# Performance work log

Hardware: AMD Instinct MI355X
Metric: run time of the kernel (lower is better)

Reference implementation:

```python
import jax, jax.numpy as jnp
import numpy as np

NUM_HEADS = 16
NEG_INF = -1e30


def setup_inputs() -> dict:
    key = jax.random.key(0)
    ks = jax.random.split(key, 12)
    T, B, E = 1024, 8, 1024
    H = NUM_HEADS
    hd = E // H
    gain = 1.0 / np.sqrt(2.0)
    # xavier_uniform bound for [E, E] weight
    bound = np.sqrt(6.0 / (E + E))
    inp = {
        "query": jax.random.normal(ks[0], (T, B, E), jnp.float32),
        "key": jax.random.normal(ks[1], (T, B, E), jnp.float32),
        "value": jax.random.normal(ks[2], (T, B, E), jnp.float32),
        "key_padding_mask": jnp.zeros((B, T), dtype=bool),  # no padding
        "attn_mask": jnp.triu(jnp.ones((T, T), dtype=bool), k=1),  # causal
        "Wq": jax.random.uniform(ks[3], (E, E), jnp.float32, -bound * gain, bound * gain),
        "bq": jnp.zeros((E,), jnp.float32),
        "Wk": jax.random.uniform(ks[4], (E, E), jnp.float32, -bound * gain, bound * gain),
        "bk": jnp.zeros((E,), jnp.float32),
        "Wv": jax.random.uniform(ks[5], (E, E), jnp.float32, -bound * gain, bound * gain),
        "bv": jnp.zeros((E,), jnp.float32),
        "Wo": jax.random.uniform(ks[6], (E, E), jnp.float32, -bound, bound),
        "bo": jnp.zeros((E,), jnp.float32),
    }
    return inp


def reference(query, key, value, key_padding_mask, attn_mask,
              Wq, bq, Wk, bk, Wv, bv, Wo, bo):
    T, B, E = query.shape
    H = NUM_HEADS
    hd = E // H
    scaling = hd ** -0.5
    S = key.shape[0]

    # projections (nn.Linear: x @ W.T + b)
    q = (query @ Wq.T + bq) * scaling          # [T, B, E]
    k = key @ Wk.T + bk                         # [S, B, E]
    v = value @ Wv.T + bv                       # [S, B, E]

    # -> [B*H, len, hd] (fairseq layout)
    q = q.reshape(T, B * H, hd).transpose(1, 0, 2)
    k = k.reshape(S, B * H, hd).transpose(1, 0, 2)
    v = v.reshape(S, B * H, hd).transpose(1, 0, 2)

    scores = jnp.einsum('nth,nsh->nts', q, k)   # [B*H, T, S]
    scores = jnp.where(attn_mask[None, :, :], NEG_INF, scores)
    scores = scores.reshape(B, H, T, S)
    scores = jnp.where(key_padding_mask[:, None, None, :], NEG_INF, scores)

    # fp32 softmax (matches softmax(..., dtype=torch.float32))
    weights = jax.nn.softmax(scores.astype(jnp.float32), axis=-1)  # [B, H, T, S]

    # dropout p=0.0 in eval -> identity
    probs = weights.reshape(B * H, T, S)
    attn = jnp.einsum('nts,nsh->nth', probs, v)  # [B*H, T, hd]
    attn = attn.transpose(1, 0, 2).reshape(T, B, E)
    attn = attn @ Wo.T + bo                      # [T, B, E]

    avg_weights = jnp.sum(weights, axis=1) / H   # [B, T, S]
    return attn, avg_weights, weights
```

## Files before the change

### kernel.cpp

```cpp
#include <hip/hip_runtime.h>
#include <hip/hip_bf16.h>
#include <stdint.h>

typedef unsigned short u16;
typedef __attribute__((ext_vector_type(8))) short bf16x8;
typedef __attribute__((ext_vector_type(4))) float f32x4;

#define LDS_AS __attribute__((address_space(3)))
#define GLB_AS __attribute__((address_space(1)))


__device__ __forceinline__ u16 f2bf(float f) {
  union { float f; uint32_t u; } v; v.f = f;
  uint32_t u = v.u;
  u += 0x7FFFu + ((u >> 16) & 1u);
  return (u16)(u >> 16);
}

__device__ __forceinline__ f32x4 mfma16(bf16x8 a, bf16x8 b, f32x4 c) {
  return __builtin_amdgcn_mfma_f32_16x16x32_bf16(a, b, c, 0, 0, 0);
}

__device__ __forceinline__ void gll16(const void* g, void* l) {
  __builtin_amdgcn_global_load_lds((const GLB_AS void*)(uintptr_t)g,
                                   (LDS_AS void*)(uintptr_t)l, 16, 0, 0);
}

__global__ __launch_bounds__(256) void k_cvt_all(
    const float* __restrict__ a0, const float* __restrict__ a1, const float* __restrict__ a2,
    const float* __restrict__ w0, const float* __restrict__ w1,
    const float* __restrict__ w2, const float* __restrict__ w3,
    u16* __restrict__ da0, u16* __restrict__ da1, u16* __restrict__ da2,
    u16* __restrict__ dw0, u16* __restrict__ dw1, u16* __restrict__ dw2, u16* __restrict__ dw3)
{
  int gid = blockIdx.x;
  const float* s; u16* d; int idx;
  if (gid < 24576) {
    int seg = gid >> 13; idx = gid & 8191;
    s = seg == 0 ? a0 : (seg == 1 ? a1 : a2);
    d = seg == 0 ? da0 : (seg == 1 ? da1 : da2);
  } else {
    int g2 = gid - 24576;
    int seg = g2 >> 10; idx = g2 & 1023;
    s = seg == 0 ? w0 : (seg == 1 ? w1 : (seg == 2 ? w2 : w3));
    d = seg == 0 ? dw0 : (seg == 1 ? dw1 : (seg == 2 ? dw2 : dw3));
  }
  int i = (idx * 256 + threadIdx.x) * 4;
  float4 v = *reinterpret_cast<const float4*>(s + i);
  ushort4 o;
  o.x = f2bf(v.x); o.y = f2bf(v.y); o.z = f2bf(v.z); o.w = f2bf(v.w);
  *reinterpret_cast<ushort4*>(d + i) = o;
}

__device__ __forceinline__ void gemm_core(
    const u16* __restrict__ A, const u16* __restrict__ Bw,
    const float* __restrict__ bias, void* __restrict__ outp,
    float scale, bool fp32out)
{
  __shared__ u16 aLds[128 * 64];
  __shared__ u16 bLds[128 * 64];
  const int tid = threadIdx.x;
  const int w = tid >> 6, lane = tid & 63;
  const int fr = lane & 15, fh = lane >> 4;
  const int m0 = blockIdx.x * 128, n0 = blockIdx.y * 128;
  const int wr = w >> 1, wc = w & 1;
  const int srow = tid >> 3, scol = (tid & 7) * 8;

  f32x4 zero4 = {0.f, 0.f, 0.f, 0.f};
  f32x4 acc[4][4];
#pragma unroll
  for (int i = 0; i < 4; i++)
#pragma unroll
    for (int j = 0; j < 4; j++) acc[i][j] = zero4;

  const u16* ag = A + (size_t)(m0 + srow) * 1024 + scol;
  const u16* bg = Bw + (size_t)(n0 + srow) * 1024 + scol;

  for (int k0 = 0; k0 < 1024; k0 += 64) {
#pragma unroll
    for (int it = 0; it < 4; ++it) {
      gll16(ag + (size_t)it * 32 * 1024 + k0, aLds + it * 2048 + w * 512);
      gll16(bg + (size_t)it * 32 * 1024 + k0, bLds + it * 2048 + w * 512);
    }
    __syncthreads();
#pragma unroll
    for (int ks = 0; ks < 2; ++ks) {
      bf16x8 af[4], bfr[4];
#pragma unroll
      for (int mi = 0; mi < 4; mi++)
        af[mi] = *reinterpret_cast<const bf16x8*>(&aLds[(wr * 64 + mi * 16 + fr) * 64 + ks * 32 + fh * 8]);
#pragma unroll
      for (int nj = 0; nj < 4; nj++)
        bfr[nj] = *reinterpret_cast<const bf16x8*>(&bLds[(wc * 64 + nj * 16 + fr) * 64 + ks * 32 + fh * 8]);
#pragma unroll
      for (int mi = 0; mi < 4; mi++)
#pragma unroll
        for (int nj = 0; nj < 4; nj++)
          acc[mi][nj] = mfma16(af[mi], bfr[nj], acc[mi][nj]);
    }
    __syncthreads();
  }

#pragma unroll
  for (int nj = 0; nj < 4; nj++) {
    int j = n0 + wc * 64 + nj * 16 + fr;
    float bj = bias[j];
#pragma unroll
    for (int mi = 0; mi < 4; mi++) {
#pragma unroll
      for (int r = 0; r < 4; r++) {
        int i = m0 + wr * 64 + mi * 16 + fh * 4 + r;
        float v = acc[mi][nj][r] + bj;
        if (fp32out) {
          ((float*)outp)[(size_t)i * 1024 + j] = v;
        } else {
          v *= scale;
          int t = i >> 3, b = i & 7;
          int h = j >> 6, d = j & 63;
          ((u16*)outp)[((size_t)((b * 16 + h) * 1024 + t)) * 64 + d] = f2bf(v);
        }
      }
    }
  }
}

__global__ __launch_bounds__(256) void k_gemm_qkv(
    const u16* __restrict__ xq, const u16* __restrict__ xk, const u16* __restrict__ xv,
    const u16* __restrict__ wq, const u16* __restrict__ wk, const u16* __restrict__ wv,
    const float* __restrict__ bq, const float* __restrict__ bk, const float* __restrict__ bv,
    u16* __restrict__ qo, u16* __restrict__ ko, u16* __restrict__ vo)
{
  int z = blockIdx.z;
  const u16* A = z == 0 ? xq : (z == 1 ? xk : xv);
  const u16* Bw = z == 0 ? wq : (z == 1 ? wk : wv);
  const float* bias = z == 0 ? bq : (z == 1 ? bk : bv);
  u16* o = z == 0 ? qo : (z == 1 ? ko : vo);
  float scale = z == 0 ? 0.125f : 1.0f;
  gemm_core(A, Bw, bias, o, scale, false);
}

__global__ __launch_bounds__(256) void k_gemm_o(
    const u16* __restrict__ A, const u16* __restrict__ Bw,
    const float* __restrict__ bias, float* __restrict__ outp)
{
  gemm_core(A, Bw, bias, outp, 1.0f, true);
}

__global__ __launch_bounds__(256) void k_transpose(const u16* __restrict__ vb, u16* __restrict__ vt) {
  __shared__ u16 tile[64][72];
  int n = blockIdx.y, t0 = blockIdx.x * 64;
  int tid = threadIdx.x;
  int r = tid >> 2, c0 = (tid & 3) * 16;
  const u16* src = vb + ((size_t)n * 1024 + t0 + r) * 64 + c0;
#pragma unroll
  for (int ii = 0; ii < 16; ++ii) tile[c0 + ii][r] = src[ii];
  __syncthreads();
  int d = tid >> 2;
  u16* dst = vt + ((size_t)(n * 64) + d) * 1024 + t0 + c0;
  *reinterpret_cast<uint4*>(dst)     = *reinterpret_cast<const uint4*>(&tile[d][c0]);
  *reinterpret_cast<uint4*>(dst + 8) = *reinterpret_cast<const uint4*>(&tile[d][c0 + 8]);
}

__device__ __forceinline__ void attn_step(
    const u16* lds_k, u16* lds_p, const bf16x8 (&vf)[2][4],
    int sb, int tb_, int w, int fr, int fh,
    bf16x8 qf0, bf16x8 qf1,
    f32x4 (&oacc)[4], float (&m4)[4], float (&l4)[4])
{
  int t0 = tb_ * 64 + w * 16;
  f32x4 dd[4];
#pragma unroll
  for (int ss = 0; ss < 4; ++ss) {
    int row = ss * 16 + fr;
    const u16* kr = lds_k + row * 64;
    int c0 = (fh * 16) ^ ((row & 7) << 4);
    int c1 = (64 + fh * 16) ^ ((row & 7) << 4);
    bf16x8 kf0 = *reinterpret_cast<const bf16x8*>(kr + (c0 >> 1));
    bf16x8 kf1 = *reinterpret_cast<const bf16x8*>(kr + (c1 >> 1));
    f32x4 z = {0.f, 0.f, 0.f, 0.f};
    z = mfma16(qf0, kf0, z);
    dd[ss] = mfma16(qf1, kf1, z);
  }
  if (sb == tb_) {
#pragma unroll
    for (int ss = 0; ss < 4; ++ss) {
      int s_c = sb * 64 + ss * 16 + fr;
#pragma unroll
      for (int r = 0; r < 4; ++r)
        if (s_c > t0 + fh * 4 + r) dd[ss][r] = -3.0e38f;
    }
  }
  float mn[4], scale[4];
#pragma unroll
  for (int r = 0; r < 4; ++r) {
    float bm = fmaxf(fmaxf(dd[0][r], dd[1][r]), fmaxf(dd[2][r], dd[3][r]));
#pragma unroll
    for (int bmk = 1; bmk < 16; bmk <<= 1)
      bm = fmaxf(bm, __shfl_xor(bm, bmk, 64));
    mn[r] = fmaxf(m4[r], bm);
    scale[r] = __expf(m4[r] - mn[r]);
    m4[r] = mn[r];
  }
#pragma unroll
  for (int ss = 0; ss < 4; ++ss) {
#pragma unroll
    for (int r = 0; r < 4; ++r) {
      float p = __expf(dd[ss][r] - mn[r]);
      dd[ss][r] = p;
      int row = fh * 4 + r;
      int cb = ((ss * 16 + fr) * 2) ^ ((row & 7) << 4);
      lds_p[row * 64 + (cb >> 1)] = f2bf(p);
    }
  }
#pragma unroll
  for (int r = 0; r < 4; ++r) {
    float s = (dd[0][r] + dd[1][r]) + (dd[2][r] + dd[3][r]);
#pragma unroll
    for (int bmk = 1; bmk < 16; bmk <<= 1)
      s += __shfl_xor(s, bmk, 64);
    l4[r] = l4[r] * scale[r] + s;
#pragma unroll
    for (int db = 0; db < 4; ++db) oacc[db][r] *= scale[r];
  }
  asm volatile("s_waitcnt lgkmcnt(0)" ::: "memory");
  __builtin_amdgcn_sched_barrier(0);
#pragma unroll
  for (int ks = 0; ks < 2; ++ks) {
    int pc = (ks * 64 + fh * 16) ^ ((fr & 7) << 4);
    bf16x8 pa = *reinterpret_cast<const bf16x8*>(lds_p + fr * 64 + (pc >> 1));
#pragma unroll
    for (int db = 0; db < 4; ++db)
      oacc[db] = mfma16(pa, vf[ks][db], oacc[db]);
  }
}

__global__ __launch_bounds__(256) void k_attn(
    const u16* __restrict__ qb, const u16* __restrict__ kb, const u16* __restrict__ vt,
    float* __restrict__ m_ws, float* __restrict__ l_ws, u16* __restrict__ attn_pre)
{
  __shared__ u16 kT[2][64 * 64];
  __shared__ u16 pT[4][16 * 64];
  int tid = threadIdx.x, w = tid >> 6, lane = tid & 63;
  int fr = lane & 15, fh = lane >> 4;
  int n = blockIdx.x, j = blockIdx.y;
  int tbH = 15 - j, tbL = j;
  const u16* kb_n = kb + (size_t)n * 1024 * 64;
  const u16* vt_n = vt + (size_t)n * 64 * 1024;

  bf16x8 qfH0, qfH1, qfL0, qfL1;
  {
    const u16* q = qb + ((size_t)n * 1024 + tbH * 64 + w * 16 + fr) * 64;
    qfH0 = *reinterpret_cast<const bf16x8*>(q + fh * 8);
    qfH1 = *reinterpret_cast<const bf16x8*>(q + 32 + fh * 8);
    q = qb + ((size_t)n * 1024 + tbL * 64 + w * 16 + fr) * 64;
    qfL0 = *reinterpret_cast<const bf16x8*>(q + fh * 8);
    qfL1 = *reinterpret_cast<const bf16x8*>(q + 32 + fh * 8);
  }
  f32x4 oaccH[4], oaccL[4];
  float mH[4], lH[4], mL[4], lL[4];
#pragma unroll
  for (int i = 0; i < 4; ++i) {
    oaccH[i] = (f32x4){0.f, 0.f, 0.f, 0.f};
    oaccL[i] = (f32x4){0.f, 0.f, 0.f, 0.f};
    mH[i] = -3.0e38f; lH[i] = 0.f; mL[i] = -3.0e38f; lL[i] = 0.f;
  }

  auto stage = [&](int buf, int sb) {
#pragma unroll
    for (int it = 0; it < 2; ++it) {
      int rbase = w * 16 + it * 8;
      int row = rbase + (lane >> 3);
      int colb = ((lane & 7) * 16) ^ ((lane >> 3) << 4);
      const u16* src = kb_n + ((size_t)(sb * 64 + row)) * 64 + (colb >> 1);
      gll16(src, &kT[buf][rbase * 64]);
    }
  };

  stage(0, 0);
  asm volatile("s_waitcnt vmcnt(0)" ::: "memory");
  __syncthreads();
  int cur = 0;
  for (int sb = 0; sb <= tbH; ++sb) {
    if (sb < tbH) stage(cur ^ 1, sb + 1);
    bf16x8 vf[2][4];
#pragma unroll
    for (int ks = 0; ks < 2; ++ks)
#pragma unroll
      for (int db = 0; db < 4; ++db)
        vf[ks][db] = *reinterpret_cast<const bf16x8*>(
            vt_n + ((size_t)(db * 16 + fr)) * 1024 + sb * 64 + ks * 32 + fh * 8);
    attn_step(kT[cur], pT[w], vf, sb, tbH, w, fr, fh, qfH0, qfH1, oaccH, mH, lH);
    if (sb <= tbL)
      attn_step(kT[cur], pT[w], vf, sb, tbL, w, fr, fh, qfL0, qfL1, oaccL, mL, lL);
    asm volatile("s_waitcnt vmcnt(0)" ::: "memory");
    __syncthreads();
    cur ^= 1;
  }

  int b_ = n >> 4, h_ = n & 15;
  {
    int t0 = tbH * 64 + w * 16;
    if (fr == 0) {
#pragma unroll
      for (int r = 0; r < 4; ++r) {
        m_ws[n * 1024 + t0 + fh * 4 + r] = mH[r];
        l_ws[n * 1024 + t0 + fh * 4 + r] = lH[r];
      }
    }
#pragma unroll
    for (int db = 0; db < 4; ++db)
#pragma unroll
      for (int r = 0; r < 4; ++r)
        attn_pre[((size_t)((t0 + fh * 4 + r) * 8 + b_)) * 1024 + h_ * 64 + db * 16 + fr] =
            f2bf(oaccH[db][r] / lH[r]);
  }
  {
    int t0 = tbL * 64 + w * 16;
    if (fr == 0) {
#pragma unroll
      for (int r = 0; r < 4; ++r) {
        m_ws[n * 1024 + t0 + fh * 4 + r] = mL[r];
        l_ws[n * 1024 + t0 + fh * 4 + r] = lL[r];
      }
    }
#pragma unroll
    for (int db = 0; db < 4; ++db)
#pragma unroll
      for (int r = 0; r < 4; ++r)
        attn_pre[((size_t)((t0 + fh * 4 + r) * 8 + b_)) * 1024 + h_ * 64 + db * 16 + fr] =
            f2bf(oaccL[db][r] / lL[r]);
  }
}

__global__ __launch_bounds__(512) void k_weights(
    const u16* __restrict__ qb, const u16* __restrict__ kb,
    const float* __restrict__ m_ws, const float* __restrict__ l_ws,
    float* __restrict__ wout, float* __restrict__ avg)
{
  __shared__ u16 kT[2][512 * 64];
  const float L2E = 1.4426950408889634f;
  int pid = blockIdx.x;
  int b = pid >> 5, pr = pid & 31;
  int tid = threadIdx.x;
  int w = tid >> 6, lane = tid & 63, fr = lane & 15, fh = lane >> 4;
  f32x4 zero4 = {0.f, 0.f, 0.f, 0.f};

  int pA = pr, pB = 63 - pr;
  int t0A = pA * 16, t0B = pB * 16;

  f32x4 avgA[8], avgB[8];
#pragma unroll
  for (int i = 0; i < 8; ++i) { avgA[i] = zero4; avgB[i] = zero4; }

  const int srow8 = lane >> 3;
  const int scolb = ((lane & 7) * 16) ^ (srow8 << 4);

  auto stage = [&](int buf, int cc) {
    const u16* kb_n = kb + (size_t)(b * 16 + (cc >> 1)) * 65536;
    int base = (cc & 1) * 512;
#pragma unroll
    for (int j = 0; j < 8; ++j) {
      int rbase = j * 64 + w * 8;
      const u16* src = kb_n + ((size_t)(base + rbase + srow8)) * 64 + (scolb >> 1);
      gll16(src, &kT[buf][rbase * 64]);
    }
  };

  stage(0, 0);
  int cur = 0;

  for (int h = 0; h < 16; ++h) {
    int n = b * 16 + h;
    const u16* qrA = qb + ((size_t)n * 1024 + t0A + fr) * 64;
    const u16* qrB = qb + ((size_t)n * 1024 + t0B + fr) * 64;
    bf16x8 qA0 = *reinterpret_cast<const bf16x8*>(qrA + fh * 8);
    bf16x8 qA1 = *reinterpret_cast<const bf16x8*>(qrA + 32 + fh * 8);
    bf16x8 qB0 = *reinterpret_cast<const bf16x8*>(qrB + fh * 8);
    bf16x8 qB1 = *reinterpret_cast<const bf16x8*>(qrB + 32 + fh * 8);
    float cA = -m_ws[n * 1024 + t0A + fr] * L2E - __log2f(l_ws[n * 1024 + t0A + fr]);
    float cB = -m_ws[n * 1024 + t0B + fr] * L2E - __log2f(l_ws[n * 1024 + t0B + fr]);
    float* wrowA = wout + ((size_t)n << 20) + ((size_t)t0A << 10);
    float* wrowB = wout + ((size_t)n << 20) + ((size_t)t0B << 10);

#pragma unroll
    for (int kh = 0; kh < 2; ++kh) {
      int cc = h * 2 + kh;
      __builtin_amdgcn_s_barrier();
      __builtin_amdgcn_sched_barrier(0);
      if (cc < 31) stage(cur ^ 1, cc + 1);
      __builtin_amdgcn_sched_barrier(0);
      asm volatile("s_waitcnt vmcnt(8)" ::: "memory");
      __builtin_amdgcn_s_barrier();
      __builtin_amdgcn_sched_barrier(0);

      const u16* kbuf_l = kT[cur];
#pragma unroll
      for (int i = 0; i < 4; ++i) {
        int sl = w + 8 * i;
        int sg = kh * 32 + sl;
        int rowl = sl * 16 + fr;
        const u16* kr = &kbuf_l[rowl * 64];
        int c0 = (fh * 16) ^ ((rowl & 7) << 4);
        int c1 = (64 + fh * 16) ^ ((rowl & 7) << 4);
        bf16x8 kf0 = *reinterpret_cast<const bf16x8*>(kr + (c0 >> 1));
        bf16x8 kf1 = *reinterpret_cast<const bf16x8*>(kr + (c1 >> 1));

        {
          f32x4 dd = zero4;
          dd = mfma16(kf0, qA0, dd);
          dd = mfma16(kf1, qA1, dd);
          f32x4 wv;
#pragma unroll
          for (int rr = 0; rr < 4; ++rr) {
            bool valid = (sg < pA) | ((sg == pA) & (fh * 4 + rr <= fr));
            wv[rr] = valid ? __builtin_amdgcn_exp2f(dd[rr] * L2E + cA) : 0.f;
          }
          avgA[kh * 4 + i] += wv;
          *reinterpret_cast<f32x4*>(wrowA + (size_t)fr * 1024 + sg * 16 + fh * 4) = wv;
        }
        {
          f32x4 dd = zero4;
          dd = mfma16(kf0, qB0, dd);
          dd = mfma16(kf1, qB1, dd);
          f32x4 wv;
#pragma unroll
          for (int rr = 0; rr < 4; ++rr) {
            bool valid = (sg < pB) | ((sg == pB) & (fh * 4 + rr <= fr));
            wv[rr] = valid ? __builtin_amdgcn_exp2f(dd[rr] * L2E + cB) : 0.f;
          }
          avgB[kh * 4 + i] += wv;
          *reinterpret_cast<f32x4*>(wrowB + (size_t)fr * 1024 + sg * 16 + fh * 4) = wv;
        }
      }
      cur ^= 1;
    }
  }

  float* arowA = avg + (((size_t)b << 10) + t0A) * 1024;
  float* arowB = avg + (((size_t)b << 10) + t0B) * 1024;
#pragma unroll
  for (int i = 0; i < 8; ++i) {
    int sg = (i >> 2) * 32 + (w + 8 * (i & 3));
    f32x4 vA = avgA[i], vB = avgB[i];
#pragma unroll
    for (int rr = 0; rr < 4; ++rr) { vA[rr] *= 0.0625f; vB[rr] *= 0.0625f; }
    *reinterpret_cast<f32x4*>(arowA + (size_t)fr * 1024 + sg * 16 + fh * 4) = vA;
    *reinterpret_cast<f32x4*>(arowB + (size_t)fr * 1024 + sg * 16 + fh * 4) = vB;
  }
}

extern "C" void kernel_launch(void* const* d_in, const int* in_sizes, int n_in,
                              void* d_out, int out_size, void* d_ws, size_t ws_size,
                              hipStream_t stream)
{
  const float* query = (const float*)d_in[0];
  const float* key_  = (const float*)d_in[1];
  const float* value = (const float*)d_in[2];
  const float* Wq = (const float*)d_in[5];
  const float* bq = (const float*)d_in[6];
  const float* Wk = (const float*)d_in[7];
  const float* bk = (const float*)d_in[8];
  const float* Wv = (const float*)d_in[9];
  const float* bv = (const float*)d_in[10];
  const float* Wo = (const float*)d_in[11];
  const float* bo = (const float*)d_in[12];

  char* ws = (char*)d_ws;
  size_t off = 0;
  auto alloc = [&](size_t bytes) { char* p = ws + off; off += (bytes + 255) & ~255ull; return p; };

  u16* xq   = (u16*)alloc(8192ull * 1024 * 2);
  u16* xk   = (u16*)alloc(8192ull * 1024 * 2);
  u16* xv   = (u16*)alloc(8192ull * 1024 * 2);
  u16* wqb  = (u16*)alloc(1024ull * 1024 * 2);
  u16* wkb  = (u16*)alloc(1024ull * 1024 * 2);
  u16* wvb  = (u16*)alloc(1024ull * 1024 * 2);
  u16* wob  = (u16*)alloc(1024ull * 1024 * 2);
  u16* qbuf = (u16*)alloc(128ull * 1024 * 64 * 2);
  u16* kbuf = (u16*)alloc(128ull * 1024 * 64 * 2);
  u16* vbuf = (u16*)alloc(128ull * 1024 * 64 * 2);
  u16* vtb  = (u16*)alloc(128ull * 64 * 1024 * 2);
  u16* apre = (u16*)alloc(8192ull * 1024 * 2);
  float* mws = (float*)alloc(128ull * 1024 * 4);
  float* lws = (float*)alloc(128ull * 1024 * 4);

  float* out_attn = (float*)d_out;
  float* out_avg  = out_attn + 8388608;
  float* out_w    = out_avg + 8388608;

  k_cvt_all<<<28672, 256, 0, stream>>>(query, key_, value, Wq, Wk, Wv, Wo,
                                       xq, xk, xv, wqb, wkb, wvb, wob);

  k_gemm_qkv<<<dim3(64, 8, 3), 256, 0, stream>>>(xq, xk, xv, wqb, wkb, wvb,
                                                 bq, bk, bv, qbuf, kbuf, vbuf);

  k_transpose<<<dim3(16, 128), 256, 0, stream>>>(vbuf, vtb);
  k_attn<<<dim3(128, 8), 256, 0, stream>>>(qbuf, kbuf, vtb, mws, lws, apre);
  k_weights<<<256, 512, 0, stream>>>(qbuf, kbuf, mws, lws, out_w, out_avg);
  k_gemm_o<<<dim3(64, 8), 256, 0, stream>>>(apre, wob, bo, out_attn);
}
```

Measured before the change: 408.8 us.

## Split weights kernel to one query tile per block and pipeline attn K staging

k_weights now gives each block a single 16-row query tile instead of a balanced pair, and doubles the grid to 512 blocks. K is staged in 256-row quarters with a smaller LDS footprint, and the vmcnt waits are tuned to match. Separately, k_attn replaces its full vmcnt(0)+syncthreads at the end of each iteration with barrier/partial-wait double buffering, so the next K block loads while the current one is computed. The weights kernel still computes all 1024 key columns per row, so the old causal load-balance pairing is unnecessary. More blocks raise occupancy, but each block now re-stages K once per query tile, which doubles K reads.

Measured after the change: 453.5 us. +10.9%, slower.

```diff
diff --git a/kernel.cpp b/kernel.cpp
--- a/kernel.cpp
+++ b/kernel.cpp
@@ -277,11 +277,8 @@
   };
 
   stage(0, 0);
-  asm volatile("s_waitcnt vmcnt(0)" ::: "memory");
-  __syncthreads();
   int cur = 0;
   for (int sb = 0; sb <= tbH; ++sb) {
-    if (sb < tbH) stage(cur ^ 1, sb + 1);
     bf16x8 vf[2][4];
 #pragma unroll
     for (int ks = 0; ks < 2; ++ks)
@@ -289,11 +286,21 @@
       for (int db = 0; db < 4; ++db)
         vf[ks][db] = *reinterpret_cast<const bf16x8*>(
             vt_n + ((size_t)(db * 16 + fr)) * 1024 + sb * 64 + ks * 32 + fh * 8);
+    __builtin_amdgcn_s_barrier();
+    __builtin_amdgcn_sched_barrier(0);
+    if (sb < tbH) {
+      stage(cur ^ 1, sb + 1);
+      __builtin_amdgcn_sched_barrier(0);
+      asm volatile("s_waitcnt vmcnt(10)" ::: "memory");
+    } else {
+      asm volatile("s_waitcnt vmcnt(8)" ::: "memory");
+    }
+    __builtin_amdgcn_s_barrier();
+    __builtin_amdgcn_sched_barrier(0);
+
     attn_step(kT[cur], pT[w], vf, sb, tbH, w, fr, fh, qfH0, qfH1, oaccH, mH, lH);
     if (sb <= tbL)
       attn_step(kT[cur], pT[w], vf, sb, tbL, w, fr, fh, qfL0, qfL1, oaccL, mL, lL);
-    asm volatile("s_waitcnt vmcnt(0)" ::: "memory");
-    __syncthreads();
     cur ^= 1;
   }
 
@@ -337,30 +344,28 @@
     const float* __restrict__ m_ws, const float* __restrict__ l_ws,
     float* __restrict__ wout, float* __restrict__ avg)
 {
-  __shared__ u16 kT[2][512 * 64];
+  __shared__ u16 kT[2][256 * 64];
   const float L2E = 1.4426950408889634f;
   int pid = blockIdx.x;
-  int b = pid >> 5, pr = pid & 31;
+  int b = pid >> 6, p = pid & 63;
+  int t0 = p * 16;
   int tid = threadIdx.x;
   int w = tid >> 6, lane = tid & 63, fr = lane & 15, fh = lane >> 4;
   f32x4 zero4 = {0.f, 0.f, 0.f, 0.f};
 
-  int pA = pr, pB = 63 - pr;
-  int t0A = pA * 16, t0B = pB * 16;
-
-  f32x4 avgA[8], avgB[8];
-#pragma unroll
-  for (int i = 0; i < 8; ++i) { avgA[i] = zero4; avgB[i] = zero4; }
+  f32x4 avga[8];
+#pragma unroll
+  for (int i = 0; i < 8; ++i) avga[i] = zero4;
 
   const int srow8 = lane >> 3;
   const int scolb = ((lane & 7) * 16) ^ (srow8 << 4);
 
   auto stage = [&](int buf, int cc) {
-    const u16* kb_n = kb + (size_t)(b * 16 + (cc >> 1)) * 65536;
-    int base = (cc & 1) * 512;
-#pragma unroll
-    for (int j = 0; j < 8; ++j) {
-      int rbase = j * 64 + w * 8;
+    const u16* kb_n = kb + (size_t)(b * 16 + (cc >> 2)) * 65536;
+    int base = (cc & 3) * 256;
+#pragma unroll
+    for (int jj = 0; jj < 4; ++jj) {
+      int rbase = jj * 64 + w * 8;
       const u16* src = kb_n + ((size_t)(base + rbase + srow8)) * 64 + (scolb >> 1);
       gll16(src, &kT[buf][rbase * 64]);
     }
@@ -369,35 +374,42 @@
   stage(0, 0);
   int cur = 0;
 
+  bf16x8 q0, q1;
+  float ch;
+  float* wrow = nullptr;
+
   for (int h = 0; h < 16; ++h) {
     int n = b * 16 + h;
-    const u16* qrA = qb + ((size_t)n * 1024 + t0A + fr) * 64;
-    const u16* qrB = qb + ((size_t)n * 1024 + t0B + fr) * 64;
-    bf16x8 qA0 = *reinterpret_cast<const bf16x8*>(qrA + fh * 8);
-    bf16x8 qA1 = *reinterpret_cast<const bf16x8*>(qrA + 32 + fh * 8);
-    bf16x8 qB0 = *reinterpret_cast<const bf16x8*>(qrB + fh * 8);
-    bf16x8 qB1 = *reinterpret_cast<const bf16x8*>(qrB + 32 + fh * 8);
-    float cA = -m_ws[n * 1024 + t0A + fr] * L2E - __log2f(l_ws[n * 1024 + t0A + fr]);
-    float cB = -m_ws[n * 1024 + t0B + fr] * L2E - __log2f(l_ws[n * 1024 + t0B + fr]);
-    float* wrowA = wout + ((size_t)n << 20) + ((size_t)t0A << 10);
-    float* wrowB = wout + ((size_t)n << 20) + ((size_t)t0B << 10);
-
-#pragma unroll
-    for (int kh = 0; kh < 2; ++kh) {
-      int cc = h * 2 + kh;
+#pragma unroll
+    for (int qt = 0; qt < 4; ++qt) {
+      int cc = h * 4 + qt;
       __builtin_amdgcn_s_barrier();
       __builtin_amdgcn_sched_barrier(0);
-      if (cc < 31) stage(cur ^ 1, cc + 1);
+      if (cc < 63) stage(cur ^ 1, cc + 1);
       __builtin_amdgcn_sched_barrier(0);
-      asm volatile("s_waitcnt vmcnt(8)" ::: "memory");
+      if (qt == 0 && h == 0) {
+        asm volatile("s_waitcnt vmcnt(4)" ::: "memory");
+      } else if (qt == 3 && h == 15) {
+        asm volatile("s_waitcnt vmcnt(2)" ::: "memory");
+      } else {
+        asm volatile("s_waitcnt vmcnt(6)" ::: "memory");
+      }
       __builtin_amdgcn_s_barrier();
       __builtin_amdgcn_sched_barrier(0);
 
+      if (qt == 0) {
+        const u16* qr = qb + ((size_t)n * 1024 + t0 + fr) * 64;
+        q0 = *reinterpret_cast<const bf16x8*>(qr + fh * 8);
+        q1 = *reinterpret_cast<const bf16x8*>(qr + 32 + fh * 8);
+        ch = -m_ws[n * 1024 + t0 + fr] * L2E - __log2f(l_ws[n * 1024 + t0 + fr]);
+        wrow = wout + ((size_t)n << 20) + ((size_t)t0 << 10);
+      }
+
       const u16* kbuf_l = kT[cur];
 #pragma unroll
-      for (int i = 0; i < 4; ++i) {
-        int sl = w + 8 * i;
-        int sg = kh * 32 + sl;
+      for (int i = 0; i < 2; ++i) {
+        int sl = w * 2 + i;
+        int sg = qt * 16 + sl;
         int rowl = sl * 16 + fr;
         const u16* kr = &kbuf_l[rowl * 64];
         int c0 = (fh * 16) ^ ((rowl & 7) << 4);
@@ -405,48 +417,33 @@
         bf16x8 kf0 = *reinterpret_cast<const bf16x8*>(kr + (c0 >> 1));
         bf16x8 kf1 = *reinterpret_cast<const bf16x8*>(kr + (c1 >> 1));
 
-        {
-          f32x4 dd = zero4;
-          dd = mfma16(kf0, qA0, dd);
-          dd = mfma16(kf1, qA1, dd);
-          f32x4 wv;
-#pragma unroll
-          for (int rr = 0; rr < 4; ++rr) {
-            bool valid = (sg < pA) | ((sg == pA) & (fh * 4 + rr <= fr));
-            wv[rr] = valid ? __builtin_amdgcn_exp2f(dd[rr] * L2E + cA) : 0.f;
-          }
-          avgA[kh * 4 + i] += wv;
-          *reinterpret_cast<f32x4*>(wrowA + (size_t)fr * 1024 + sg * 16 + fh * 4) = wv;
+        f32x4 dd = zero4;
+        dd = mfma16(kf0, q0, dd);
+        dd = mfma16(kf1, q1, dd);
+        f32x4 wv;
+#pragma unroll
+        for (int rr = 0; rr < 4; ++rr) {
+          bool valid = (sg < p) | ((sg == p) & (fh * 4 + rr <= fr));
+          wv[rr] = valid ? __builtin_amdgcn_exp2f(dd[rr] * L2E + ch) : 0.f;
         }
-        {
-          f32x4 dd = zero4;
-          dd = mfma16(kf0, qB0, dd);
-          dd = mfma16(kf1, qB1, dd);
-          f32x4 wv;
-#pragma unroll
-          for (int rr = 0; rr < 4; ++rr) {
-            bool valid = (sg < pB) | ((sg == pB) & (fh * 4 + rr <= fr));
-            wv[rr] = valid ? __builtin_amdgcn_exp2f(dd[rr] * L2E + cB) : 0.f;
-          }
-          avgB[kh * 4 + i] += wv;
-          *reinterpret_cast<f32x4*>(wrowB + (size_t)fr * 1024 + sg * 16 + fh * 4) = wv;
-        }
+        avga[qt * 2 + i] += wv;
+        *reinterpret_cast<f32x4*>(wrow + (size_t)fr * 1024 + sg * 16 + fh * 4) = wv;
       }
       cur ^= 1;
     }
   }
 
-  float* arowA = avg + (((size_t)b << 10) + t0A) * 1024;
-  float* arowB = avg + (((size_t)b << 10) + t0B) * 1024;
-#pragma unroll
-  for (int i = 0; i < 8; ++i) {
-    int sg = (i >> 2) * 32 + (w + 8 * (i & 3));
-    f32x4 vA = avgA[i], vB = avgB[i];
-#pragma unroll
-    for (int rr = 0; rr < 4; ++rr) { vA[rr] *= 0.0625f; vB[rr] *= 0.0625f; }
-    *reinterpret_cast<f32x4*>(arowA + (size_t)fr * 1024 + sg * 16 + fh * 4) = vA;
-    *reinterpret_cast<f32x4*>(arowB + (size_t)fr * 1024 + sg * 16 + fh * 4) = vB;
-  }
+  float* arow = avg + (((size_t)b << 10) + t0) * 1024;
+#pragma unroll
+  for (int qt = 0; qt < 4; ++qt)
+#pragma unroll
+    for (int i = 0; i < 2; ++i) {
+      int sg = qt * 16 + w * 2 + i;
+      f32x4 v = avga[qt * 2 + i];
+#pragma unroll
+      for (int rr = 0; rr < 4; ++rr) v[rr] *= 0.0625f;
+      *reinterpret_cast<f32x4*>(arow + (size_t)fr * 1024 + sg * 16 + fh * 4) = v;
+    }
 }
 
 extern "C" void kernel_launch(void* const* d_in, const int* in_sizes, int n_in,
@@ -496,6 +493,6 @@
 
   k_transpose<<<dim3(16, 128), 256, 0, stream>>>(vbuf, vtb);
   k_attn<<<dim3(128, 8), 256, 0, stream>>>(qbuf, kbuf, vtb, mws, lws, apre);
-  k_weights<<<256, 512, 0, stream>>>(qbuf, kbuf, mws, lws, out_w, out_avg);
+  k_weights<<<512, 512, 0, stream>>>(qbuf, kbuf, mws, lws, out_w, out_avg);
   k_gemm_o<<<dim3(64, 8), 256, 0, stream>>>(apre, wob, bo, out_attn);
 }
```
